# Kernel optimization log

Measured on AMD Instinct MI355X. Metric: run time of the kernel, lower is better.

The kernel has to match this reference:

```python
import jax, jax.numpy as jnp
import numpy as np

B, NQ, NC, D, H = 4, 4096, 4096, 1024, 16
HD = D // H
LN_EPS = 1e-5


def _layernorm(x, g, b):
    mu = jnp.mean(x, axis=-1, keepdims=True)
    var = jnp.var(x, axis=-1, keepdims=True)
    return (x - mu) * jax.lax.rsqrt(var + LN_EPS) * g + b


def _kernel(x):
    # elu(x) + 1  (strictly positive feature map)
    return jax.nn.elu(x) + 1.0


def setup_inputs() -> dict:
    key = jax.random.key(0)
    ks = jax.random.split(key, 12)
    s = 1.0 / np.sqrt(D)
    return {
        "query": jax.random.normal(ks[0], (B, NQ, D), jnp.float32),
        "context": jax.random.normal(ks[1], (B, NC, D), jnp.float32),
        "q_w": jax.random.uniform(ks[2], (D, D), jnp.float32, -s, s),
        "q_b": jnp.zeros((D,), jnp.float32),
        "k_w": jax.random.uniform(ks[3], (D, D), jnp.float32, -s, s),
        "k_b": jnp.zeros((D,), jnp.float32),
        "v_w": jax.random.uniform(ks[4], (D, D), jnp.float32, -s, s),
        "v_b": jnp.zeros((D,), jnp.float32),
        "o_w": jax.random.uniform(ks[5], (D, D), jnp.float32, -s, s),
        "o_b": jnp.zeros((D,), jnp.float32),
        "lnq_g": jnp.ones((D,), jnp.float32),
        "lnq_b": jnp.zeros((D,), jnp.float32),
        "lnkv_g": jnp.ones((D,), jnp.float32),
        "lnkv_b": jnp.zeros((D,), jnp.float32),
    }


def reference(query, context, q_w, q_b, k_w, k_b, v_w, v_b, o_w, o_b,
              lnq_g, lnq_b, lnkv_g, lnkv_b):
    residual = query
    q = _layernorm(query, lnq_g, lnq_b)
    c = _layernorm(context, lnkv_g, lnkv_b)

    # torch Linear: y = x @ W.T + b ; reshape to (B, H, N, Hd)
    Q = (q @ q_w.T + q_b).reshape(B, NQ, H, HD).transpose(0, 2, 1, 3)
    K = (c @ k_w.T + k_b).reshape(B, NC, H, HD).transpose(0, 2, 1, 3)
    V = (c @ v_w.T + v_b).reshape(B, NC, H, HD).transpose(0, 2, 1, 3)

    Q = _kernel(Q)
    K = _kernel(K)

    # KV: (B, H, Hd, Hd) outer-product accumulation over context length
    KV = jnp.einsum("bhnd,bhne->bhde", K, V)
    K_sum = K.sum(axis=2)                              # (B, H, Hd)
    Z = jnp.einsum("bhqd,bhd->bhq", Q, K_sum)          # (B, H, Nq)
    Z = jnp.maximum(Z, 1e-6)

    out = jnp.einsum("bhqd,bhde->bhqe", Q, KV) / Z[..., None]
    out = out.transpose(0, 2, 1, 3).reshape(B, NQ, D)
    return residual + (out @ o_w.T + o_b)
```

## Files before the change

### kernel.cpp

```cpp
#include <hip/hip_runtime.h>

#define DEV __device__ __forceinline__

typedef __attribute__((ext_vector_type(8))) short short8;
typedef __attribute__((ext_vector_type(4))) short short4v;
typedef __attribute__((ext_vector_type(4))) float f32x4;

DEV float bf2f(unsigned short u) { return __uint_as_float(((unsigned int)u) << 16); }
DEV unsigned short f2bf(float f) {
    unsigned int u = __float_as_uint(f);
    u += 0x7FFFu + ((u >> 16) & 1u);
    return (unsigned short)(u >> 16);
}

DEV float elu1(float v) { return v > 0.0f ? v + 1.0f : __expf(v); }

DEV void gload_lds16(const void* g, void* l) {
    __builtin_amdgcn_global_load_lds(
        (__attribute__((address_space(1))) unsigned int*)(g),
        (__attribute__((address_space(3))) unsigned int*)(l),
        16, 0, 0);
}

#define NROW 16384
#define DDIM 1024

__global__ __launch_bounds__(256) void ln_kernel(
    const float* __restrict__ query, const float* __restrict__ context,
    const float* __restrict__ lnq_g, const float* __restrict__ lnq_b,
    const float* __restrict__ lnk_g, const float* __restrict__ lnk_b,
    unsigned short* __restrict__ qln, unsigned short* __restrict__ cln)
{
    const int row = blockIdx.x;
    const bool isq = row < NROW;
    const int r = isq ? row : row - NROW;
    const float* src = (isq ? query : context) + (size_t)r * DDIM;
    const float* g   = isq ? lnq_g : lnk_g;
    const float* bb  = isq ? lnq_b : lnk_b;
    unsigned short* dst = (isq ? qln : cln) + (size_t)r * DDIM;

    const int tid = threadIdx.x;
    f32x4 x = *(const f32x4*)(src + tid * 4);
    float s  = x[0] + x[1] + x[2] + x[3];
    float sq = x[0]*x[0] + x[1]*x[1] + x[2]*x[2] + x[3]*x[3];
#pragma unroll
    for (int off = 32; off; off >>= 1) {
        s  += __shfl_xor(s, off);
        sq += __shfl_xor(sq, off);
    }
    __shared__ float red[8];
    const int lane = tid & 63, w = tid >> 6;
    if (lane == 0) { red[w] = s; red[4 + w] = sq; }
    __syncthreads();
    s  = red[0] + red[1] + red[2] + red[3];
    sq = red[4] + red[5] + red[6] + red[7];
    const float mu  = s * (1.0f / DDIM);
    const float var = sq * (1.0f / DDIM) - mu * mu;
    const float rstd = rsqrtf(var + 1e-5f);

    f32x4 gv = *(const f32x4*)(g + tid * 4);
    f32x4 bv = *(const f32x4*)(bb + tid * 4);
    short4v o;
#pragma unroll
    for (int j = 0; j < 4; ++j)
        o[j] = (short)f2bf((x[j] - mu) * rstd * gv[j] + bv[j]);
    *(short4v*)(dst + tid * 4) = o;
}

__global__ __launch_bounds__(256) void conv_w(
    const float* __restrict__ a, const float* __restrict__ b,
    const float* __restrict__ c, const float* __restrict__ d,
    unsigned short* __restrict__ out)
{
    const int i = blockIdx.x * 256 + threadIdx.x;
    const int mat = i >> 18;
    const int idx = (i & 262143) * 4;
    const float* src = mat == 0 ? a : mat == 1 ? b : mat == 2 ? c : d;
    f32x4 v = *(const f32x4*)(src + idx);
    short4v o;
#pragma unroll
    for (int j = 0; j < 4; ++j) o[j] = (short)f2bf(v[j]);
    *(short4v*)(out + (size_t)mat * 1048576 + idx) = o;
}

template <typename EPI>
DEV void gemm128(unsigned short* __restrict__ sA,
                 unsigned short* __restrict__ sB,
                 const unsigned short* __restrict__ Ap,
                 const unsigned short* __restrict__ Bp,
                 int m0, int n0, EPI epi)
{
    const int tid = threadIdx.x;
    const int lane = tid & 63, w = tid >> 6;
    const int wr = w >> 1, wc = w & 1;
    const int lr = lane & 15, lg = lane >> 4;

    const int srow = tid >> 2, sch = tid & 3;
    const unsigned short* gA0 = Ap + (size_t)(m0 + srow) * 1024 + sch * 8;
    const unsigned short* gB0 = Bp + (size_t)(n0 + srow) * 1024 + sch * 8;
    unsigned short* dA = sA + tid * 8;
    unsigned short* dB = sB + tid * 8;

    f32x4 acc[4][4];
#pragma unroll
    for (int i = 0; i < 4; ++i)
#pragma unroll
        for (int j = 0; j < 4; ++j)
#pragma unroll
            for (int e = 0; e < 4; ++e) acc[i][j][e] = 0.0f;

    for (int t = 0; t < 32; ++t) {
        const int ko = t * 32;
        gload_lds16(gA0 + ko, dA);
        gload_lds16(gA0 + ko + (size_t)65536, dA + 2048);
        gload_lds16(gB0 + ko, dB);
        gload_lds16(gB0 + ko + (size_t)65536, dB + 2048);
        asm volatile("s_waitcnt vmcnt(0)" ::: "memory");
        __syncthreads();

        short8 af[4], bf[4];
#pragma unroll
        for (int mt = 0; mt < 4; ++mt)
            af[mt] = *(const short8*)&sA[(wr * 64 + mt * 16 + lr) * 32 + lg * 8];
#pragma unroll
        for (int nt = 0; nt < 4; ++nt)
            bf[nt] = *(const short8*)&sB[(wc * 64 + nt * 16 + lr) * 32 + lg * 8];
#pragma unroll
        for (int mt = 0; mt < 4; ++mt)
#pragma unroll
            for (int nt = 0; nt < 4; ++nt)
                acc[mt][nt] = __builtin_amdgcn_mfma_f32_16x16x32_bf16(
                    af[mt], bf[nt], acc[mt][nt], 0, 0, 0);
        __syncthreads();
    }

#pragma unroll
    for (int mt = 0; mt < 4; ++mt)
#pragma unroll
        for (int nt = 0; nt < 4; ++nt) {
            const int col = n0 + wc * 64 + nt * 16 + lr;
#pragma unroll
            for (int i = 0; i < 4; ++i) {
                const int row = m0 + wr * 64 + mt * 16 + lg * 4 + i;
                epi(row, col, acc[mt][nt][i]);
            }
        }
}

__global__ __launch_bounds__(256, 4) void gemm_qkv(
    const unsigned short* __restrict__ QLN, const unsigned short* __restrict__ WQ,
    const unsigned short* __restrict__ CLN, const unsigned short* __restrict__ WKV,
    unsigned short* __restrict__ Qm, unsigned short* __restrict__ KVT,
    const float* __restrict__ q_b, const float* __restrict__ k_b,
    const float* __restrict__ v_b)
{
    __shared__ __attribute__((aligned(16))) unsigned short sA[128 * 32];
    __shared__ __attribute__((aligned(16))) unsigned short sB[128 * 32];

    const int bid = blockIdx.x;
    const int l = (bid & 7) * 384 + (bid >> 3);

    if (l < 1024) {
        const int m0 = (l >> 3) * 128, n0 = (l & 7) * 128;
        gemm128(sA, sB, QLN, WQ, m0, n0,
            [&](int row, int col, float v) {
                v = elu1(v + q_b[col]);
                Qm[(size_t)row * 1024 + col] = f2bf(v);
            });
    } else {
        const int r = l - 1024;
        const int m0 = (r & 15) * 128, n0 = (r >> 4) * 128;
        gemm128(sA, sB, WKV, CLN, m0, n0,
            [&](int row, int col, float v) {
                if (row < 1024) v = elu1(v + k_b[row]);
                else            v = v + v_b[row - 1024];
                KVT[(size_t)row * NROW + col] = f2bf(v);
            });
    }
}

__global__ __launch_bounds__(256, 4) void gemm_out(
    const unsigned short* __restrict__ A2, const unsigned short* __restrict__ WO,
    float* __restrict__ Out, const float* __restrict__ o_b,
    const float* __restrict__ resid)
{
    __shared__ __attribute__((aligned(16))) unsigned short sA[128 * 32];
    __shared__ __attribute__((aligned(16))) unsigned short sB[128 * 32];

    const int bid = blockIdx.x;
    const int l = (bid & 7) * 128 + (bid >> 3);
    const int m0 = (l >> 3) * 128, n0 = (l & 7) * 128;
    gemm128(sA, sB, A2, WO, m0, n0,
        [&](int row, int col, float v) {
            Out[(size_t)row * 1024 + col] =
                v + o_b[col] + resid[(size_t)row * 1024 + col];
        });
}

__global__ __launch_bounds__(256) void kv_kernel(
    const unsigned short* __restrict__ VT, const unsigned short* __restrict__ KT,
    float* __restrict__ KVTp)
{
    const int bh = blockIdx.x, sp = blockIdx.y;
    const int b = bh >> 4, h = bh & 15;
    const int tid = threadIdx.x, lane = tid & 63, w = tid >> 6;
    const int lr = lane & 15, lg = lane >> 4;

    f32x4 acc[4][4];
#pragma unroll
    for (int i = 0; i < 4; ++i)
#pragma unroll
        for (int j = 0; j < 4; ++j)
#pragma unroll
            for (int e = 0; e < 4; ++e) acc[i][j][e] = 0.0f;

    const size_t colbase = (size_t)b * 4096 + sp * 1024 + w * 256 + lg * 8;
    const unsigned short* va = VT + (size_t)(h * 64 + lr) * NROW + colbase;
    const unsigned short* ka = KT + (size_t)(h * 64 + lr) * NROW + colbase;

    for (int ks = 0; ks < 8; ++ks) {
        short8 af[4], bfv[4];
#pragma unroll
        for (int mt = 0; mt < 4; ++mt)
            af[mt] = *(const short8*)(va + (size_t)mt * 16 * NROW + ks * 32);
#pragma unroll
        for (int nt = 0; nt < 4; ++nt)
            bfv[nt] = *(const short8*)(ka + (size_t)nt * 16 * NROW + ks * 32);
#pragma unroll
        for (int mt = 0; mt < 4; ++mt)
#pragma unroll
            for (int nt = 0; nt < 4; ++nt)
                acc[mt][nt] = __builtin_amdgcn_mfma_f32_16x16x32_bf16(
                    af[mt], bfv[nt], acc[mt][nt], 0, 0, 0);
    }

    __shared__ float red4[4][4096];
#pragma unroll
    for (int mt = 0; mt < 4; ++mt)
#pragma unroll
        for (int nt = 0; nt < 4; ++nt)
#pragma unroll
            for (int i = 0; i < 4; ++i)
                red4[w][(mt * 16 + lg * 4 + i) * 64 + nt * 16 + lr] = acc[mt][nt][i];
    __syncthreads();
    float* out = KVTp + ((size_t)sp * 64 + bh) * 4096;
    for (int i = tid; i < 4096; i += 256)
        out[i] = red4[0][i] + red4[1][i] + red4[2][i] + red4[3][i];
}

__global__ __launch_bounds__(256) void ksum_kernel(
    const unsigned short* __restrict__ KT, float* __restrict__ Ksum)
{
    const int bh = blockIdx.x, quad = blockIdx.y;
    const int b = bh >> 4, h = bh & 15;
    const int tid = threadIdx.x, lane = tid & 63, w = tid >> 6;
    const int dbase = quad * 16 + w * 4;
#pragma unroll
    for (int dd = 0; dd < 4; ++dd) {
        const int d = dbase + dd;
        const unsigned short* p = KT + (size_t)(h * 64 + d) * NROW + b * 4096 + lane * 8;
        float s = 0.0f;
#pragma unroll
        for (int it = 0; it < 8; ++it) {
            short8 v = *(const short8*)(p + it * 512);
#pragma unroll
            for (int j = 0; j < 8; ++j) s += bf2f((unsigned short)v[j]);
        }
#pragma unroll
        for (int off = 32; off; off >>= 1) s += __shfl_xor(s, off);
        if (lane == 0) Ksum[bh * 64 + d] = s;
    }
}

__global__ __launch_bounds__(256) void z_kernel(
    const unsigned short* __restrict__ Q, const float* __restrict__ Ksum,
    float* __restrict__ invZ)
{
    const int gid = blockIdx.x * 256 + threadIdx.x;
    const int n = gid >> 4, h = gid & 15;
    const int b = n >> 12;
    const unsigned short* q = Q + (size_t)n * DDIM + h * 64;
    const float* ks = Ksum + ((b << 4) + h) * 64;
    float z = 0.0f;
#pragma unroll
    for (int it = 0; it < 8; ++it) {
        short8 v = *(const short8*)(q + it * 8);
#pragma unroll
        for (int j = 0; j < 8; ++j) z += bf2f((unsigned short)v[j]) * ks[it * 8 + j];
    }
    invZ[gid] = 1.0f / fmaxf(z, 1e-6f);
}

__global__ __launch_bounds__(256) void a2_kernel(
    const unsigned short* __restrict__ Q, const float* __restrict__ KVTp,
    const float* __restrict__ invZ, unsigned short* __restrict__ A2)
{
    const int m0 = blockIdx.x * 128, h = blockIdx.y;
    const int b = m0 >> 12, bh = (b << 4) + h;
    const int tid = threadIdx.x, lane = tid & 63, w = tid >> 6;
    const int wr = w >> 1, wc = w & 1;
    const int lr = lane & 15, lg = lane >> 4;

    f32x4 acc[4][2];
#pragma unroll
    for (int i = 0; i < 4; ++i)
#pragma unroll
        for (int j = 0; j < 2; ++j)
#pragma unroll
            for (int e = 0; e < 4; ++e) acc[i][j][e] = 0.0f;

    const unsigned short* qa = Q + (size_t)(m0 + wr * 64 + lr) * DDIM + h * 64 + lg * 8;
    const float* kvb = KVTp + (size_t)bh * 4096 + (wc * 32 + lr) * 64 + lg * 8;

#pragma unroll
    for (int ks = 0; ks < 2; ++ks) {
        short8 af[4];
#pragma unroll
        for (int mt = 0; mt < 4; ++mt)
            af[mt] = *(const short8*)(qa + (size_t)mt * 16 * DDIM + ks * 32);
        short8 bfv[2];
#pragma unroll
        for (int nt = 0; nt < 2; ++nt) {
            const float* p = kvb + nt * 16 * 64 + ks * 32;
            short8 t;
#pragma unroll
            for (int j = 0; j < 8; ++j) {
                float v = p[j] + p[j + 262144] + p[j + 2 * 262144] + p[j + 3 * 262144];
                t[j] = (short)f2bf(v);
            }
            bfv[nt] = t;
        }
#pragma unroll
        for (int mt = 0; mt < 4; ++mt)
#pragma unroll
            for (int nt = 0; nt < 2; ++nt)
                acc[mt][nt] = __builtin_amdgcn_mfma_f32_16x16x32_bf16(
                    af[mt], bfv[nt], acc[mt][nt], 0, 0, 0);
    }

#pragma unroll
    for (int mt = 0; mt < 4; ++mt)
#pragma unroll
        for (int nt = 0; nt < 2; ++nt)
#pragma unroll
            for (int i = 0; i < 4; ++i) {
                const int row = m0 + wr * 64 + mt * 16 + lg * 4 + i;
                const int col = h * 64 + wc * 32 + nt * 16 + lr;
                const float v = acc[mt][nt][i] * invZ[row * 16 + h];
                A2[(size_t)row * DDIM + col] = f2bf(v);
            }
}

extern "C" void kernel_launch(void* const* d_in, const int* in_sizes, int n_in,
                              void* d_out, int out_size, void* d_ws, size_t ws_size,
                              hipStream_t stream)
{
    const float* query   = (const float*)d_in[0];
    const float* context = (const float*)d_in[1];
    const float* q_w = (const float*)d_in[2];
    const float* q_b = (const float*)d_in[3];
    const float* k_w = (const float*)d_in[4];
    const float* k_b = (const float*)d_in[5];
    const float* v_w = (const float*)d_in[6];
    const float* v_b = (const float*)d_in[7];
    const float* o_w = (const float*)d_in[8];
    const float* o_b = (const float*)d_in[9];
    const float* lnq_g = (const float*)d_in[10];
    const float* lnq_b = (const float*)d_in[11];
    const float* lnk_g = (const float*)d_in[12];
    const float* lnk_b = (const float*)d_in[13];

    char* ws = (char*)d_ws;
    unsigned short* WQ  = (unsigned short*)(ws);
    unsigned short* WKV = (unsigned short*)(ws + (2u << 20));
    unsigned short* WO  = (unsigned short*)(ws + (6u << 20));
    unsigned short* QLN = (unsigned short*)(ws + (8u << 20));
    unsigned short* CLN = (unsigned short*)(ws + (40u << 20));
    unsigned short* Qm  = (unsigned short*)(ws + (72u << 20));
    unsigned short* KT  = (unsigned short*)(ws + (104u << 20));
    unsigned short* VT  = (unsigned short*)(ws + (136u << 20));
    float* KVTp = (float*)(ws + (168u << 20));
    float* Ksum = (float*)(ws + (172u << 20));
    float* invZ = (float*)(ws + (173u << 20));
    unsigned short* A2 = QLN;

    conv_w<<<4096, 256, 0, stream>>>(q_w, k_w, v_w, o_w, WQ);
    ln_kernel<<<2 * NROW, 256, 0, stream>>>(query, context, lnq_g, lnq_b,
                                            lnk_g, lnk_b, QLN, CLN);
    gemm_qkv<<<3072, 256, 0, stream>>>(QLN, WQ, CLN, WKV, Qm, KT,
                                       q_b, k_b, v_b);
    kv_kernel<<<dim3(64, 4), 256, 0, stream>>>(VT, KT, KVTp);
    ksum_kernel<<<dim3(64, 4), 256, 0, stream>>>(KT, Ksum);
    z_kernel<<<1024, 256, 0, stream>>>(Qm, Ksum, invZ);
    a2_kernel<<<dim3(128, 16), 256, 0, stream>>>(Qm, KVTp, invZ, A2);
    gemm_out<<<1024, 256, 0, stream>>>(A2, WO, (float*)d_out, o_b, query);
}
```

Before: 326.3 us.

## Pipeline GEMM K-loop with swizzled LDS and fuse K-sum into kv kernel

The shared GEMM routine now stages a BK=64 tile using an XOR-swizzled LDS layout, which is meant to cut bank conflicts. It issues the next tile's global-to-LDS loads after the second-half fragment reads, so loads overlap the second MFMA batch, and it raises wave priority around MFMAs. The column sum of K is fused into kv_kernel as per-split partial sums that z_kernel adds up, removing the separate ksum_kernel pass over K. LDS per block doubles, which may lower occupancy, and the single-buffer reuse depends on careful barrier and waitcnt placement.

```diff
diff --git a/kernel.cpp b/kernel.cpp
--- a/kernel.cpp
+++ b/kernel.cpp
@@ -95,12 +95,16 @@
     const int wr = w >> 1, wc = w & 1;
     const int lr = lane & 15, lg = lane >> 4;
 
-    const int srow = tid >> 2, sch = tid & 3;
-    const unsigned short* gA0 = Ap + (size_t)(m0 + srow) * 1024 + sch * 8;
-    const unsigned short* gB0 = Bp + (size_t)(n0 + srow) * 1024 + sch * 8;
+    const int srow = tid >> 3;
+    const int cswz = (tid & 7) ^ (srow & 7);
+    const unsigned short* gA0 = Ap + (size_t)(m0 + srow) * 1024 + cswz * 8;
+    const unsigned short* gB0 = Bp + (size_t)(n0 + srow) * 1024 + cswz * 8;
     unsigned short* dA = sA + tid * 8;
     unsigned short* dB = sB + tid * 8;
 
+    const int sw0 = ((0 + lg) ^ (lr & 7)) * 8;
+    const int sw1 = ((4 + lg) ^ (lr & 7)) * 8;
+
     f32x4 acc[4][4];
 #pragma unroll
     for (int i = 0; i < 4; ++i)
@@ -109,30 +113,56 @@
 #pragma unroll
             for (int e = 0; e < 4; ++e) acc[i][j][e] = 0.0f;
 
-    for (int t = 0; t < 32; ++t) {
-        const int ko = t * 32;
-        gload_lds16(gA0 + ko, dA);
-        gload_lds16(gA0 + ko + (size_t)65536, dA + 2048);
-        gload_lds16(gB0 + ko, dB);
-        gload_lds16(gB0 + ko + (size_t)65536, dB + 2048);
+#define STG8(T)                                                               \
+    {                                                                         \
+        const int ko = (T) * 64;                                              \
+        _Pragma("unroll")                                                     \
+        for (int j = 0; j < 4; ++j) {                                         \
+            gload_lds16(gA0 + ko + (size_t)j * 32768, dA + j * 2048);         \
+            gload_lds16(gB0 + ko + (size_t)j * 32768, dB + j * 2048);         \
+        }                                                                     \
+    }
+
+    STG8(0);
+    for (int t = 0; t < 16; ++t) {
         asm volatile("s_waitcnt vmcnt(0)" ::: "memory");
-        __syncthreads();
+        __builtin_amdgcn_s_barrier();
 
         short8 af[4], bf[4];
 #pragma unroll
         for (int mt = 0; mt < 4; ++mt)
-            af[mt] = *(const short8*)&sA[(wr * 64 + mt * 16 + lr) * 32 + lg * 8];
+            af[mt] = *(const short8*)&sA[(wr * 64 + mt * 16 + lr) * 64 + sw0];
 #pragma unroll
         for (int nt = 0; nt < 4; ++nt)
-            bf[nt] = *(const short8*)&sB[(wc * 64 + nt * 16 + lr) * 32 + lg * 8];
+            bf[nt] = *(const short8*)&sB[(wc * 64 + nt * 16 + lr) * 64 + sw0];
+        __builtin_amdgcn_s_setprio(1);
 #pragma unroll
         for (int mt = 0; mt < 4; ++mt)
 #pragma unroll
             for (int nt = 0; nt < 4; ++nt)
                 acc[mt][nt] = __builtin_amdgcn_mfma_f32_16x16x32_bf16(
                     af[mt], bf[nt], acc[mt][nt], 0, 0, 0);
-        __syncthreads();
-    }
+        __builtin_amdgcn_s_setprio(0);
+
+#pragma unroll
+        for (int mt = 0; mt < 4; ++mt)
+            af[mt] = *(const short8*)&sA[(wr * 64 + mt * 16 + lr) * 64 + sw1];
+#pragma unroll
+        for (int nt = 0; nt < 4; ++nt)
+            bf[nt] = *(const short8*)&sB[(wc * 64 + nt * 16 + lr) * 64 + sw1];
+        asm volatile("s_waitcnt lgkmcnt(0)" ::: "memory");
+        __builtin_amdgcn_s_barrier();
+        if (t < 15) STG8(t + 1);
+        __builtin_amdgcn_s_setprio(1);
+#pragma unroll
+        for (int mt = 0; mt < 4; ++mt)
+#pragma unroll
+            for (int nt = 0; nt < 4; ++nt)
+                acc[mt][nt] = __builtin_amdgcn_mfma_f32_16x16x32_bf16(
+                    af[mt], bf[nt], acc[mt][nt], 0, 0, 0);
+        __builtin_amdgcn_s_setprio(0);
+    }
+#undef STG8
 
 #pragma unroll
     for (int mt = 0; mt < 4; ++mt)
@@ -154,8 +184,8 @@
     const float* __restrict__ q_b, const float* __restrict__ k_b,
     const float* __restrict__ v_b)
 {
-    __shared__ __attribute__((aligned(16))) unsigned short sA[128 * 32];
-    __shared__ __attribute__((aligned(16))) unsigned short sB[128 * 32];
+    __shared__ __attribute__((aligned(16))) unsigned short sA[128 * 64];
+    __shared__ __attribute__((aligned(16))) unsigned short sB[128 * 64];
 
     const int bid = blockIdx.x;
     const int l = (bid & 7) * 384 + (bid >> 3);
@@ -184,8 +214,8 @@
     float* __restrict__ Out, const float* __restrict__ o_b,
     const float* __restrict__ resid)
 {
-    __shared__ __attribute__((aligned(16))) unsigned short sA[128 * 32];
-    __shared__ __attribute__((aligned(16))) unsigned short sB[128 * 32];
+    __shared__ __attribute__((aligned(16))) unsigned short sA[128 * 64];
+    __shared__ __attribute__((aligned(16))) unsigned short sB[128 * 64];
 
     const int bid = blockIdx.x;
     const int l = (bid & 7) * 128 + (bid >> 3);
@@ -199,7 +229,7 @@
 
 __global__ __launch_bounds__(256) void kv_kernel(
     const unsigned short* __restrict__ VT, const unsigned short* __restrict__ KT,
-    float* __restrict__ KVTp)
+    float* __restrict__ KVTp, float* __restrict__ Ksump)
 {
     const int bh = blockIdx.x, sp = blockIdx.y;
     const int b = bh >> 4, h = bh & 15;
@@ -213,6 +243,7 @@
         for (int j = 0; j < 4; ++j)
 #pragma unroll
             for (int e = 0; e < 4; ++e) acc[i][j][e] = 0.0f;
+    float kp[4] = {0.0f, 0.0f, 0.0f, 0.0f};
 
     const size_t colbase = (size_t)b * 4096 + sp * 1024 + w * 256 + lg * 8;
     const unsigned short* va = VT + (size_t)(h * 64 + lr) * NROW + colbase;
@@ -232,6 +263,22 @@
             for (int nt = 0; nt < 4; ++nt)
                 acc[mt][nt] = __builtin_amdgcn_mfma_f32_16x16x32_bf16(
                     af[mt], bfv[nt], acc[mt][nt], 0, 0, 0);
+#pragma unroll
+        for (int nt = 0; nt < 4; ++nt)
+#pragma unroll
+            for (int j = 0; j < 8; ++j)
+                kp[nt] += bf2f((unsigned short)bfv[nt][j]);
+    }
+
+#pragma unroll
+    for (int nt = 0; nt < 4; ++nt) {
+        kp[nt] += __shfl_xor(kp[nt], 16);
+        kp[nt] += __shfl_xor(kp[nt], 32);
+    }
+    __shared__ float kred[4][64];
+    if (lane < 16) {
+#pragma unroll
+        for (int nt = 0; nt < 4; ++nt) kred[w][nt * 16 + lane] = kp[nt];
     }
 
     __shared__ float red4[4][4096];
@@ -246,47 +293,30 @@
     float* out = KVTp + ((size_t)sp * 64 + bh) * 4096;
     for (int i = tid; i < 4096; i += 256)
         out[i] = red4[0][i] + red4[1][i] + red4[2][i] + red4[3][i];
-}
-
-__global__ __launch_bounds__(256) void ksum_kernel(
-    const unsigned short* __restrict__ KT, float* __restrict__ Ksum)
-{
-    const int bh = blockIdx.x, quad = blockIdx.y;
-    const int b = bh >> 4, h = bh & 15;
-    const int tid = threadIdx.x, lane = tid & 63, w = tid >> 6;
-    const int dbase = quad * 16 + w * 4;
-#pragma unroll
-    for (int dd = 0; dd < 4; ++dd) {
-        const int d = dbase + dd;
-        const unsigned short* p = KT + (size_t)(h * 64 + d) * NROW + b * 4096 + lane * 8;
-        float s = 0.0f;
-#pragma unroll
-        for (int it = 0; it < 8; ++it) {
-            short8 v = *(const short8*)(p + it * 512);
-#pragma unroll
-            for (int j = 0; j < 8; ++j) s += bf2f((unsigned short)v[j]);
-        }
-#pragma unroll
-        for (int off = 32; off; off >>= 1) s += __shfl_xor(s, off);
-        if (lane == 0) Ksum[bh * 64 + d] = s;
-    }
+    if (tid < 64)
+        Ksump[((size_t)sp * 64 + bh) * 64 + tid] =
+            kred[0][tid] + kred[1][tid] + kred[2][tid] + kred[3][tid];
 }
 
 __global__ __launch_bounds__(256) void z_kernel(
-    const unsigned short* __restrict__ Q, const float* __restrict__ Ksum,
+    const unsigned short* __restrict__ Q, const float* __restrict__ Ksump,
     float* __restrict__ invZ)
 {
     const int gid = blockIdx.x * 256 + threadIdx.x;
     const int n = gid >> 4, h = gid & 15;
     const int b = n >> 12;
     const unsigned short* q = Q + (size_t)n * DDIM + h * 64;
-    const float* ks = Ksum + ((b << 4) + h) * 64;
+    const float* k0 = Ksump + ((size_t)((b << 4) + h)) * 64;
     float z = 0.0f;
 #pragma unroll
     for (int it = 0; it < 8; ++it) {
         short8 v = *(const short8*)(q + it * 8);
 #pragma unroll
-        for (int j = 0; j < 8; ++j) z += bf2f((unsigned short)v[j]) * ks[it * 8 + j];
+        for (int j = 0; j < 8; ++j) {
+            const int d = it * 8 + j;
+            const float ksv = k0[d] + k0[d + 4096] + k0[d + 8192] + k0[d + 12288];
+            z += bf2f((unsigned short)v[j]) * ksv;
+        }
     }
     invZ[gid] = 1.0f / fmaxf(z, 1e-6f);
 }
@@ -379,9 +409,9 @@
     unsigned short* Qm  = (unsigned short*)(ws + (72u << 20));
     unsigned short* KT  = (unsigned short*)(ws + (104u << 20));
     unsigned short* VT  = (unsigned short*)(ws + (136u << 20));
-    float* KVTp = (float*)(ws + (168u << 20));
-    float* Ksum = (float*)(ws + (172u << 20));
-    float* invZ = (float*)(ws + (173u << 20));
+    float* KVTp  = (float*)(ws + (168u << 20));
+    float* Ksump = (float*)(ws + (172u << 20));
+    float* invZ  = (float*)(ws + (173u << 20));
     unsigned short* A2 = QLN;
 
     conv_w<<<4096, 256, 0, stream>>>(q_w, k_w, v_w, o_w, WQ);
@@ -389,9 +419,8 @@
                                             lnk_g, lnk_b, QLN, CLN);
     gemm_qkv<<<3072, 256, 0, stream>>>(QLN, WQ, CLN, WKV, Qm, KT,
                                        q_b, k_b, v_b);
-    kv_kernel<<<dim3(64, 4), 256, 0, stream>>>(VT, KT, KVTp);
-    ksum_kernel<<<dim3(64, 4), 256, 0, stream>>>(KT, Ksum);
-    z_kernel<<<1024, 256, 0, stream>>>(Qm, Ksum, invZ);
+    kv_kernel<<<dim3(64, 4), 256, 0, stream>>>(VT, KT, KVTp, Ksump);
+    z_kernel<<<1024, 256, 0, stream>>>(Qm, Ksump, invZ);
     a2_kernel<<<dim3(128, 16), 256, 0, stream>>>(Qm, KVTp, invZ, A2);
     gemm_out<<<1024, 256, 0, stream>>>(A2, WO, (float*)d_out, o_b, query);
 }
```

Result: faster. 315.7 us (-3.2%).
